# Kernel optimization log

Hardware: AMD Instinct MI355X
Metric: run time of the kernel (lower is better)

## Reference

```python
import jax, jax.numpy as jnp
import numpy as np


def setup_inputs() -> dict:
    key = jax.random.key(0)
    kx, kb, kc, ka, kd = jax.random.split(key, 5)
    B, L, D, N = 8, 4096, 1024, 128
    x = jax.random.normal(kx, (B, L, D), jnp.float32)
    B_w = jax.random.normal(kb, (N, D), jnp.float32) * 0.01  # nn.Linear(d_model->d_state).weight
    C_w = jax.random.normal(kc, (D, N), jnp.float32)         # nn.Linear(d_state->d_model).weight
    # stable negative log_A (HiPPO init gives -|diag|+0.1 < 0)
    log_A = -jax.random.uniform(ka, (N,), jnp.float32) * 3.0 - 0.1
    D_param = jax.random.normal(kd, (D,), jnp.float32)
    return dict(x=x, B_w=B_w, C_w=C_w, log_A=log_A, D_param=D_param)


def reference(x, B_w, C_w, log_A, D_param):
    # x: (B,L,D); B_w: (N,D); C_w: (D,N); log_A: (N,); D_param: (D,)
    A = jnp.exp(log_A)                                   # (N,) diagonal transition
    x_proj = jnp.einsum('bld,nd->bln', x, B_w)           # B @ x  -> (B,L,N)

    def step(h, u):                                      # h_t = A*h_{t-1} + u_t
        h = A * h + u
        return h, h

    h0 = jnp.zeros((x.shape[0], B_w.shape[0]), x.dtype)  # (B,N)
    _, hs = jax.lax.scan(step, h0, jnp.swapaxes(x_proj, 0, 1))  # hs: (L,B,N)

    y = jnp.einsum('lbn,dn->bld', hs, C_w)               # C @ h -> (B,L,D)
    y = y + x * D_param                                  # skip term D*x

    last = x_proj[:, -1, :]                              # (B,N)
    final_state = jnp.broadcast_to(last.mean(axis=0, keepdims=True), last.shape)
    return y, final_state
```

## Files before the change

### kernel.cpp

```cpp
#include <hip/hip_runtime.h>


typedef _Float16 half8 __attribute__((ext_vector_type(8)));
typedef _Float16 half4 __attribute__((ext_vector_type(4)));
typedef float f32x4 __attribute__((ext_vector_type(4)));

#define BDIM 8
#define LDIM 4096
#define DDIM 1024
#define NDIM 128
#define MTOT (BDIM * LDIM)
#define CHUNK 128
#define NCHUNK (LDIM / CHUNK)
#define TOTCHUNK (BDIM * NCHUNK)

__device__ __forceinline__ void dma16(const void* g, void* l) {
    __builtin_amdgcn_global_load_lds((const __attribute__((address_space(1))) void*)g,
                                     (__attribute__((address_space(3))) void*)l, 16, 0, 0);
}

__global__ __launch_bounds__(256) void prep(const float* __restrict__ x,
                                            const float* __restrict__ Bw,
                                            const float* __restrict__ Cw,
                                            _Float16* __restrict__ Bwh,
                                            _Float16* __restrict__ Cwh,
                                            float* __restrict__ out) {
    const int blk = blockIdx.x;
    const int t = threadIdx.x;
    if (blk < 128) {
        const int n = blk;
        float s = 0.f;
        const float* br = Bw + n * DDIM;
        for (int b = 0; b < BDIM; ++b) {
            const float* xr = x + ((size_t)b * LDIM + (LDIM - 1)) * DDIM;
            for (int k = t; k < DDIM; k += 256)
                s = fmaf(xr[k], br[k], s);
        }
        __shared__ float red[256];
        red[t] = s;
        __syncthreads();
        for (int off = 128; off > 0; off >>= 1) {
            if (t < off) red[t] += red[t + off];
            __syncthreads();
        }
        if (t == 0) {
            float v = red[0] * 0.125f;
            for (int b = 0; b < BDIM; ++b)
                out[(size_t)MTOT * DDIM + b * NDIM + n] = v;
        }
    } else {
        const int base = (blk - 128) * 4096;
#pragma unroll
        for (int j = 0; j < 4; ++j) {
            int e = base + j * 1024 + t * 4;
            const float* src;
            _Float16* dst;
            if (e < 131072) { src = Bw + e; dst = Bwh + e; }
            else            { src = Cw + (e - 131072); dst = Cwh + (e - 131072); }
            float4 v = *reinterpret_cast<const float4*>(src);
            half4 h = { (_Float16)v.x, (_Float16)v.y, (_Float16)v.z, (_Float16)v.w };
            *reinterpret_cast<half4*>(dst) = h;
        }
    }
}

__global__ __launch_bounds__(256) void gemm1(const float* __restrict__ x,
                                             const _Float16* __restrict__ Bwh,
                                             float* __restrict__ xp) {
    __shared__ _Float16 As[64 * 32];
    __shared__ _Float16 Bs[128 * 32];
    const int t = threadIdx.x;
    const int row0 = blockIdx.x * 64;
    const int wave = t >> 6, lane = t & 63;
    const int wr = (wave >> 1) * 32, wc = (wave & 1) * 64;
    const int lrow = lane & 15, kq = (lane >> 4) * 8;

    f32x4 acc[2][4] = {};

    for (int kk = 0; kk < DDIM; kk += 32) {
#pragma unroll
        for (int j = 0; j < 2; ++j) {
            int i = t + 256 * j;
            int r = i >> 3, c4 = i & 7;
            float4 v = *reinterpret_cast<const float4*>(&x[(row0 + r) * DDIM + kk + c4 * 4]);
            half4 h = { (_Float16)v.x, (_Float16)v.y, (_Float16)v.z, (_Float16)v.w };
            *reinterpret_cast<half4*>(&As[r * 32 + c4 * 4]) = h;
        }
#pragma unroll
        for (int inst = 0; inst < 2; ++inst) {
            int s = inst * 256 + t;
            int r = s >> 2, c8 = s & 3;
            dma16(&Bwh[r * DDIM + kk + c8 * 8], &Bs[(inst * 256 + wave * 64) * 8]);
        }
        __syncthreads();

        half8 bf[4];
#pragma unroll
        for (int ct = 0; ct < 4; ++ct)
            bf[ct] = *reinterpret_cast<const half8*>(&Bs[(wc + ct * 16 + lrow) * 32 + kq]);
#pragma unroll
        for (int rt = 0; rt < 2; ++rt) {
            half8 af = *reinterpret_cast<const half8*>(&As[(wr + rt * 16 + lrow) * 32 + kq]);
#pragma unroll
            for (int ct = 0; ct < 4; ++ct)
                acc[rt][ct] = __builtin_amdgcn_mfma_f32_16x16x32_f16(af, bf[ct], acc[rt][ct], 0, 0, 0);
        }
        __syncthreads();
    }

    const int q4 = (lane >> 4) * 4;
#pragma unroll
    for (int rt = 0; rt < 2; ++rt)
#pragma unroll
        for (int ct = 0; ct < 4; ++ct) {
            int col = wc + ct * 16 + lrow;
#pragma unroll
            for (int i = 0; i < 4; ++i)
                xp[(row0 + wr + rt * 16 + q4 + i) * NDIM + col] = acc[rt][ct][i];
        }
}

__global__ void scan_agg(const float* __restrict__ xp, const float* __restrict__ logA,
                         float* __restrict__ agg) {
    const int chunk = blockIdx.x;
    const int n = threadIdx.x;
    const float A = expf(logA[n]);
    const float* u = xp + chunk * CHUNK * NDIM + n;
    float h = 0.f;
#pragma unroll 4
    for (int j = 0; j < CHUNK; ++j)
        h = fmaf(A, h, u[j * NDIM]);
    agg[chunk * NDIM + n] = h;
}

__global__ void scan_carry(const float* __restrict__ agg, const float* __restrict__ logA,
                           float* __restrict__ hprev) {
    const int idx = blockIdx.x * blockDim.x + threadIdx.x;
    const int b = idx >> 7, n = idx & 127;
    const float A128 = expf(128.f * logA[n]);
    float c = 0.f;
    for (int ch = 0; ch < NCHUNK; ++ch) {
        int g = (b * NCHUNK + ch) * NDIM + n;
        hprev[g] = c;
        c = fmaf(A128, c, agg[g]);
    }
}

__global__ void scan_final(const float* __restrict__ xp, const float* __restrict__ logA,
                           const float* __restrict__ hprev, _Float16* __restrict__ hs) {
    const int chunk = blockIdx.x;
    const int n = threadIdx.x;
    const float A = expf(logA[n]);
    float h = hprev[chunk * NDIM + n];
    const float* u = xp + chunk * CHUNK * NDIM + n;
    _Float16* o = hs + chunk * CHUNK * NDIM + n;
#pragma unroll 4
    for (int j = 0; j < CHUNK; ++j) {
        h = fmaf(A, h, u[j * NDIM]);
        o[j * NDIM] = (_Float16)h;
    }
}

#define BUFW 132
__global__ __launch_bounds__(256) void gemm2(const _Float16* __restrict__ hs,
                                             const _Float16* __restrict__ Cwh,
                                             const float* __restrict__ x,
                                             const float* __restrict__ Dp,
                                             float* __restrict__ y) {
    __shared__ char smem[65536];
    __shared__ __align__(16) float DpS[128];
    _Float16* hsP = (_Float16*)smem;
    _Float16* CsP = (_Float16*)(smem + 32768);

    const int t = threadIdx.x;
    const int row0 = blockIdx.x * 128;
    const int col0 = blockIdx.y * 128;
    const int wave = t >> 6, lane = t & 63;
    const int wr = (wave >> 1) * 64, wc = (wave & 1) * 64;
    const int lrow = lane & 15, kq = (lane >> 4) * 8;

    if (t < 128) DpS[t] = Dp[col0 + t];

#pragma unroll
    for (int inst = 0; inst < 8; ++inst) {
        int s = inst * 256 + t;
        int kb = s >> 9, r = (s & 511) >> 2, c8 = s & 3;
        void* ldst = &hsP[(inst * 256 + wave * 64) * 8];
        dma16(&hs[(row0 + r) * NDIM + kb * 32 + c8 * 8], ldst);
    }
#pragma unroll
    for (int inst = 0; inst < 8; ++inst) {
        int s = inst * 256 + t;
        int kb = s >> 9, r = (s & 511) >> 2, c8 = s & 3;
        void* ldst = &CsP[(inst * 256 + wave * 64) * 8];
        dma16(&Cwh[(col0 + r) * NDIM + kb * 32 + c8 * 8], ldst);
    }
    __syncthreads();

    f32x4 acc[4][4] = {};
#pragma unroll
    for (int kb = 0; kb < 4; ++kb) {
        half8 bf[4];
#pragma unroll
        for (int ct = 0; ct < 4; ++ct)
            bf[ct] = *reinterpret_cast<const half8*>(&CsP[kb * 4096 + (wc + ct * 16 + lrow) * 32 + kq]);
#pragma unroll
        for (int rt = 0; rt < 4; ++rt) {
            half8 af = *reinterpret_cast<const half8*>(&hsP[kb * 4096 + (wr + rt * 16 + lrow) * 32 + kq]);
#pragma unroll
            for (int ct = 0; ct < 4; ++ct)
                acc[rt][ct] = __builtin_amdgcn_mfma_f32_16x16x32_f16(af, bf[ct], acc[rt][ct], 0, 0, 0);
        }
    }

    float* buf = (float*)smem;
    const int q4 = (lane >> 4) * 4;
#pragma unroll
    for (int half_ = 0; half_ < 2; ++half_) {
        __syncthreads();
        if ((wr >> 6) == half_) {
#pragma unroll
            for (int rt = 0; rt < 4; ++rt)
#pragma unroll
                for (int ct = 0; ct < 4; ++ct) {
                    int col = wc + ct * 16 + lrow;
#pragma unroll
                    for (int i = 0; i < 4; ++i)
                        buf[(rt * 16 + q4 + i) * BUFW + col] = acc[rt][ct][i];
                }
        }
        __syncthreads();
#pragma unroll
        for (int j = 0; j < 8; ++j) {
            int idx = t + 256 * j;
            int row = idx >> 5, c4 = idx & 31;
            int grow = row0 + half_ * 64 + row;
            float4 a = *reinterpret_cast<const float4*>(&buf[row * BUFW + c4 * 4]);
            float4 xv = *reinterpret_cast<const float4*>(&x[(size_t)grow * DDIM + col0 + c4 * 4]);
            float4 dp = *reinterpret_cast<const float4*>(&DpS[c4 * 4]);
            float4 o;
            o.x = a.x + xv.x * dp.x;
            o.y = a.y + xv.y * dp.y;
            o.z = a.z + xv.z * dp.z;
            o.w = a.w + xv.w * dp.w;
            *reinterpret_cast<float4*>(&y[(size_t)grow * DDIM + col0 + c4 * 4]) = o;
        }
    }
}

extern "C" void kernel_launch(void* const* d_in, const int* in_sizes, int n_in,
                              void* d_out, int out_size, void* d_ws, size_t ws_size,
                              hipStream_t stream) {
    const float* x    = (const float*)d_in[0];
    const float* Bw   = (const float*)d_in[1];
    const float* Cw   = (const float*)d_in[2];
    const float* logA = (const float*)d_in[3];
    const float* Dp   = (const float*)d_in[4];
    float* out = (float*)d_out;

    char* ws = (char*)d_ws;
    float*    xp    = (float*)   (ws);
    _Float16* hs    = (_Float16*)(ws + 16777216);
    float*    agg   = (float*)   (ws + 25165824);
    float*    hprev = (float*)   (ws + 25296896);
    _Float16* Bwh   = (_Float16*)(ws + 25427968);
    _Float16* Cwh   = (_Float16*)(ws + 25690112);

    prep<<<192, 256, 0, stream>>>(x, Bw, Cw, Bwh, Cwh, out);
    gemm1<<<MTOT / 64, 256, 0, stream>>>(x, Bwh, xp);
    scan_agg<<<TOTCHUNK, 128, 0, stream>>>(xp, logA, agg);
    scan_carry<<<4, 256, 0, stream>>>(agg, logA, hprev);
    scan_final<<<TOTCHUNK, 128, 0, stream>>>(xp, logA, hprev, hs);
    gemm2<<<dim3(MTOT / 128, DDIM / 128), 256, 0, stream>>>(hs, Cwh, x, Dp, out);
}
```

Measured before the change: 330.6 us.

## Load GEMM operands straight from global memory and shrink scan chunks

Both GEMM kernels drop LDS staging and barriers and load MFMA fragments directly from global memory into registers. gemm2 now only uses shared memory for the epilogue buffer and asks for 4 blocks per CU. The scan chunk size drops from 128 to 32, giving four times as many scan blocks for more parallelism, at the cost of a longer serial carry pass. The workspace offsets are moved to fit the larger agg and hprev arrays. Direct loads lose the cooperative, coalesced reuse that LDS gave, and each wave issues strided row-wise reads that depend on the caches.

```diff
diff --git a/kernel.cpp b/kernel.cpp
--- a/kernel.cpp
+++ b/kernel.cpp
@@ -10,14 +10,9 @@
 #define DDIM 1024
 #define NDIM 128
 #define MTOT (BDIM * LDIM)
-#define CHUNK 128
+#define CHUNK 32
 #define NCHUNK (LDIM / CHUNK)
 #define TOTCHUNK (BDIM * NCHUNK)
-
-__device__ __forceinline__ void dma16(const void* g, void* l) {
-    __builtin_amdgcn_global_load_lds((const __attribute__((address_space(1))) void*)g,
-                                     (__attribute__((address_space(3))) void*)l, 16, 0, 0);
-}
 
 __global__ __launch_bounds__(256) void prep(const float* __restrict__ x,
                                             const float* __restrict__ Bw,
@@ -67,8 +62,6 @@
 __global__ __launch_bounds__(256) void gemm1(const float* __restrict__ x,
                                              const _Float16* __restrict__ Bwh,
                                              float* __restrict__ xp) {
-    __shared__ _Float16 As[64 * 32];
-    __shared__ _Float16 Bs[128 * 32];
     const int t = threadIdx.x;
     const int row0 = blockIdx.x * 64;
     const int wave = t >> 6, lane = t & 63;
@@ -76,36 +69,29 @@
     const int lrow = lane & 15, kq = (lane >> 4) * 8;
 
     f32x4 acc[2][4] = {};
+    const float* a0 = x + (size_t)(row0 + wr + lrow) * DDIM + kq;
+    const float* a1 = a0 + 16 * DDIM;
+    const _Float16* b0 = Bwh + (size_t)(wc + lrow) * DDIM + kq;
 
     for (int kk = 0; kk < DDIM; kk += 32) {
-#pragma unroll
-        for (int j = 0; j < 2; ++j) {
-            int i = t + 256 * j;
-            int r = i >> 3, c4 = i & 7;
-            float4 v = *reinterpret_cast<const float4*>(&x[(row0 + r) * DDIM + kk + c4 * 4]);
-            half4 h = { (_Float16)v.x, (_Float16)v.y, (_Float16)v.z, (_Float16)v.w };
-            *reinterpret_cast<half4*>(&As[r * 32 + c4 * 4]) = h;
-        }
-#pragma unroll
-        for (int inst = 0; inst < 2; ++inst) {
-            int s = inst * 256 + t;
-            int r = s >> 2, c8 = s & 3;
-            dma16(&Bwh[r * DDIM + kk + c8 * 8], &Bs[(inst * 256 + wave * 64) * 8]);
-        }
-        __syncthreads();
-
         half8 bf[4];
 #pragma unroll
         for (int ct = 0; ct < 4; ++ct)
-            bf[ct] = *reinterpret_cast<const half8*>(&Bs[(wc + ct * 16 + lrow) * 32 + kq]);
+            bf[ct] = *reinterpret_cast<const half8*>(b0 + (size_t)ct * 16 * DDIM + kk);
+        half8 af[2];
 #pragma unroll
         for (int rt = 0; rt < 2; ++rt) {
-            half8 af = *reinterpret_cast<const half8*>(&As[(wr + rt * 16 + lrow) * 32 + kq]);
+            const float* ap = (rt ? a1 : a0) + kk;
+            float4 v0 = *reinterpret_cast<const float4*>(ap);
+            float4 v1 = *reinterpret_cast<const float4*>(ap + 4);
+            af[rt] = half8{ (_Float16)v0.x, (_Float16)v0.y, (_Float16)v0.z, (_Float16)v0.w,
+                            (_Float16)v1.x, (_Float16)v1.y, (_Float16)v1.z, (_Float16)v1.w };
+        }
+#pragma unroll
+        for (int rt = 0; rt < 2; ++rt)
 #pragma unroll
             for (int ct = 0; ct < 4; ++ct)
-                acc[rt][ct] = __builtin_amdgcn_mfma_f32_16x16x32_f16(af, bf[ct], acc[rt][ct], 0, 0, 0);
-        }
-        __syncthreads();
+                acc[rt][ct] = __builtin_amdgcn_mfma_f32_16x16x32_f16(af[rt], bf[ct], acc[rt][ct], 0, 0, 0);
     }
 
     const int q4 = (lane >> 4) * 4;
@@ -125,9 +111,9 @@
     const int chunk = blockIdx.x;
     const int n = threadIdx.x;
     const float A = expf(logA[n]);
-    const float* u = xp + chunk * CHUNK * NDIM + n;
+    const float* u = xp + (size_t)chunk * CHUNK * NDIM + n;
     float h = 0.f;
-#pragma unroll 4
+#pragma unroll
     for (int j = 0; j < CHUNK; ++j)
         h = fmaf(A, h, u[j * NDIM]);
     agg[chunk * NDIM + n] = h;
@@ -137,12 +123,12 @@
                            float* __restrict__ hprev) {
     const int idx = blockIdx.x * blockDim.x + threadIdx.x;
     const int b = idx >> 7, n = idx & 127;
-    const float A128 = expf(128.f * logA[n]);
+    const float Ac = expf((float)CHUNK * logA[n]);
     float c = 0.f;
     for (int ch = 0; ch < NCHUNK; ++ch) {
         int g = (b * NCHUNK + ch) * NDIM + n;
         hprev[g] = c;
-        c = fmaf(A128, c, agg[g]);
+        c = fmaf(Ac, c, agg[g]);
     }
 }
 
@@ -152,9 +138,9 @@
     const int n = threadIdx.x;
     const float A = expf(logA[n]);
     float h = hprev[chunk * NDIM + n];
-    const float* u = xp + chunk * CHUNK * NDIM + n;
-    _Float16* o = hs + chunk * CHUNK * NDIM + n;
-#pragma unroll 4
+    const float* u = xp + (size_t)chunk * CHUNK * NDIM + n;
+    _Float16* o = hs + (size_t)chunk * CHUNK * NDIM + n;
+#pragma unroll
     for (int j = 0; j < CHUNK; ++j) {
         h = fmaf(A, h, u[j * NDIM]);
         o[j * NDIM] = (_Float16)h;
@@ -162,15 +148,13 @@
 }
 
 #define BUFW 132
-__global__ __launch_bounds__(256) void gemm2(const _Float16* __restrict__ hs,
-                                             const _Float16* __restrict__ Cwh,
-                                             const float* __restrict__ x,
-                                             const float* __restrict__ Dp,
-                                             float* __restrict__ y) {
-    __shared__ char smem[65536];
+__global__ __launch_bounds__(256, 4) void gemm2(const _Float16* __restrict__ hs,
+                                                const _Float16* __restrict__ Cwh,
+                                                const float* __restrict__ x,
+                                                const float* __restrict__ Dp,
+                                                float* __restrict__ y) {
+    __shared__ float buf[64 * BUFW];
     __shared__ __align__(16) float DpS[128];
-    _Float16* hsP = (_Float16*)smem;
-    _Float16* CsP = (_Float16*)(smem + 32768);
 
     const int t = threadIdx.x;
     const int row0 = blockIdx.x * 128;
@@ -181,39 +165,26 @@
 
     if (t < 128) DpS[t] = Dp[col0 + t];
 
-#pragma unroll
-    for (int inst = 0; inst < 8; ++inst) {
-        int s = inst * 256 + t;
-        int kb = s >> 9, r = (s & 511) >> 2, c8 = s & 3;
-        void* ldst = &hsP[(inst * 256 + wave * 64) * 8];
-        dma16(&hs[(row0 + r) * NDIM + kb * 32 + c8 * 8], ldst);
-    }
-#pragma unroll
-    for (int inst = 0; inst < 8; ++inst) {
-        int s = inst * 256 + t;
-        int kb = s >> 9, r = (s & 511) >> 2, c8 = s & 3;
-        void* ldst = &CsP[(inst * 256 + wave * 64) * 8];
-        dma16(&Cwh[(col0 + r) * NDIM + kb * 32 + c8 * 8], ldst);
-    }
-    __syncthreads();
+    const _Float16* ha = hs + (size_t)(row0 + wr + lrow) * NDIM + kq;
+    const _Float16* cb = Cwh + (size_t)(col0 + wc + lrow) * NDIM + kq;
 
     f32x4 acc[4][4] = {};
 #pragma unroll
     for (int kb = 0; kb < 4; ++kb) {
-        half8 bf[4];
+        half8 bf[4], af[4];
 #pragma unroll
         for (int ct = 0; ct < 4; ++ct)
-            bf[ct] = *reinterpret_cast<const half8*>(&CsP[kb * 4096 + (wc + ct * 16 + lrow) * 32 + kq]);
-#pragma unroll
-        for (int rt = 0; rt < 4; ++rt) {
-            half8 af = *reinterpret_cast<const half8*>(&hsP[kb * 4096 + (wr + rt * 16 + lrow) * 32 + kq]);
+            bf[ct] = *reinterpret_cast<const half8*>(cb + (size_t)ct * 16 * NDIM + kb * 32);
+#pragma unroll
+        for (int rt = 0; rt < 4; ++rt)
+            af[rt] = *reinterpret_cast<const half8*>(ha + (size_t)rt * 16 * NDIM + kb * 32);
+#pragma unroll
+        for (int rt = 0; rt < 4; ++rt)
 #pragma unroll
             for (int ct = 0; ct < 4; ++ct)
-                acc[rt][ct] = __builtin_amdgcn_mfma_f32_16x16x32_f16(af, bf[ct], acc[rt][ct], 0, 0, 0);
-        }
-    }
-
-    float* buf = (float*)smem;
+                acc[rt][ct] = __builtin_amdgcn_mfma_f32_16x16x32_f16(af[rt], bf[ct], acc[rt][ct], 0, 0, 0);
+    }
+
     const int q4 = (lane >> 4) * 4;
 #pragma unroll
     for (int half_ = 0; half_ < 2; ++half_) {
@@ -262,9 +233,9 @@
     float*    xp    = (float*)   (ws);
     _Float16* hs    = (_Float16*)(ws + 16777216);
     float*    agg   = (float*)   (ws + 25165824);
-    float*    hprev = (float*)   (ws + 25296896);
-    _Float16* Bwh   = (_Float16*)(ws + 25427968);
-    _Float16* Cwh   = (_Float16*)(ws + 25690112);
+    float*    hprev = (float*)   (ws + 25690112);
+    _Float16* Bwh   = (_Float16*)(ws + 26214400);
+    _Float16* Cwh   = (_Float16*)(ws + 26476544);
 
     prep<<<192, 256, 0, stream>>>(x, Bw, Cw, Bwh, Cwh, out);
     gemm1<<<MTOT / 64, 256, 0, stream>>>(x, Bwh, xp);
```

Measured after the change: 361.7 us. +9.4%, slower.
